# Kernel optimization log

Hardware: AMD Instinct MI355X
Metric: run time of the kernel (lower is better)

The kernel has to match this reference:

```python
import jax, jax.numpy as jnp
import numpy as np

N, C_IN, H, W = 8, 32, 64, 64
C_OUT, KH, KW = 64, 3, 3
STRIDE, PADDING = 1, 1


def setup_inputs() -> dict:
    key = jax.random.key(0)
    k1, k2 = jax.random.split(key)
    x = jax.random.normal(k1, (N, C_IN, H, W), dtype=jnp.float32)
    # kaiming_normal_ on (OC, IC, KH, KW): std = sqrt(2 / fan_in), fan_in = IC*KH*KW
    std = (2.0 / (C_IN * KH * KW)) ** 0.5
    weight = jax.random.normal(k2, (C_OUT, C_IN, KH, KW), dtype=jnp.float32) * std
    return {"x": x, "weight": weight}


def _aeg_conv2d(x, weight, stride=STRIDE, padding=PADDING):
    n, c_in, h, w = x.shape
    oc, ic, kh, kw = weight.shape
    xp = jnp.pad(x, ((0, 0), (0, 0), (padding, padding), (padding, padding)))
    oh = (h - kh + 2 * padding) // stride + 1
    ow = (w - kw + 2 * padding) // stride + 1
    K = kh * kw
    # Extract patches with static slices (KH,KW small): ps[k] has shape (N, IC, OH, OW)
    ps = jnp.stack(
        [xp[:, :, dh:dh + (oh - 1) * stride + 1:stride, dw:dw + (ow - 1) * stride + 1:stride]
         for dh in range(kh) for dw in range(kw)], axis=0)  # (K, N, IC, OH, OW)
    ws = weight.reshape(oc, ic, K).transpose(2, 0, 1)        # (K, OC, IC)
    base = jnp.arange(oh)[:, None] + jnp.arange(ow)[None, :]  # i + j, shape (OH, OW)

    def step(r, inp):
        xk, yk, k = inp
        xk = xk[:, None]                       # (N, 1, IC, OH, OW)
        yk = yk[None, :, :, None, None]        # (1, OC, IC, 1, 1)
        even = ((base + k) % 2) == 0           # (OH, OW) parity of i+j+k
        # even: r = (r + x) * y ; odd: r = (r + y) * x  (matches aeg_integrate)
        r = jnp.where(even, (r + xk) * yk, (r + yk) * xk)
        return r, None

    r0 = jnp.zeros((n, oc, ic, oh, ow), dtype=x.dtype)
    r, _ = jax.lax.scan(step, r0, (ps, ws, jnp.arange(K)))
    return r.sum(axis=2)  # sum over input channels -> (N, OC, OH, OW)


def reference(x, weight):
    return _aeg_conv2d(x, weight)
```

## Files before the change

### kernel.cpp

```cpp
#include <hip/hip_runtime.h>
#include <hip/hip_bf16.h>

#define C_IN  32
#define C_OUT 64
#define HH    64
#define WW    64

typedef __attribute__((ext_vector_type(8))) short short8v;
typedef __attribute__((ext_vector_type(4))) float f32x4;

static __device__ __forceinline__ unsigned short f2bf(float f) {
    unsigned u = __builtin_bit_cast(unsigned, f);
    unsigned r = (u + 0x7FFFu + ((u >> 16) & 1u)) >> 16;
    return (unsigned short)r;
}
static __device__ __forceinline__ float bf2f(unsigned short b) {
    unsigned u = ((unsigned)b) << 16;
    return __builtin_bit_cast(float, u);
}

#define XS_IC   273
#define XS_ROW  68
#define XS_PAR  34

template<int P>
__device__ __forceinline__ void packB(const float* __restrict__ w,
                                      short8v* __restrict__ B16, int tid)
{
    int oct  = tid >> 6;
    int lane = tid & 63;
    int oc   = oct * 16 + (lane & 15);
    int icb  = (lane >> 4) * 8;

    float wv[72];
    const f32x4* src = (const f32x4*)(w + ((size_t)oc * C_IN + icb) * 9);
    #pragma unroll
    for (int i = 0; i < 18; ++i) {
        f32x4 v = src[i];
        wv[4 * i + 0] = v.x; wv[4 * i + 1] = v.y;
        wv[4 * i + 2] = v.z; wv[4 * i + 3] = v.w;
    }

    #pragma unroll
    for (int a = 0; a < 8; ++a) {
        float Ew = 1.f;
        #pragma unroll
        for (int k = 8; k >= 0; --k) {
            float wk = wv[9 * a + k];
            if (((P + k) & 1) == 0) { Ew *= wk; wv[9 * a + k] = Ew; }
            else                    { wv[9 * a + k] = wk * Ew; }
        }
    }

    #pragma unroll
    for (int k = 0; k < 9; ++k) {
        short8v vh;
        #pragma unroll
        for (int a = 0; a < 8; ++a)
            vh[a] = (short)f2bf(wv[9 * a + k]);
        B16[(k * 4 + oct) * 64 + lane] = vh;
    }
}

template<int P>
__device__ __forceinline__ void aeg_gemm(
    float (&xt)[8][9], const short8v* __restrict__ Bq, f32x4 (&acc)[4], int l)
{
    #pragma unroll
    for (int a = 0; a < 8; ++a) {
        float Ox = 1.f;
        #pragma unroll
        for (int k = 8; k >= 0; --k) {
            if (((P + k) & 1) == 1) { Ox *= xt[a][k]; xt[a][k] = Ox; }
            else                    { xt[a][k] = xt[a][k] * Ox; }
        }
    }

    #pragma unroll
    for (int t = 0; t < 4; ++t) acc[t] = (f32x4){0.f, 0.f, 0.f, 0.f};

    #pragma unroll
    for (int k = 0; k < 9; ++k) {
        short8v ah, al;
        #pragma unroll
        for (int a = 0; a < 8; ++a) {
            float v  = xt[a][k];
            __hip_bfloat16 bh = __float2bfloat16(v);
            float fh = __bfloat162float(bh);
            __hip_bfloat16 bl = __float2bfloat16(v - fh);
            ah[a] = (short)__builtin_bit_cast(unsigned short, bh);
            al[a] = (short)__builtin_bit_cast(unsigned short, bl);
        }
        #pragma unroll
        for (int t = 0; t < 4; ++t) {
            short8v bh = Bq[(k * 4 + t) * 64 + l];
            acc[t] = __builtin_amdgcn_mfma_f32_16x16x32_bf16(ah, bh, acc[t], 0, 0, 0);
            acc[t] = __builtin_amdgcn_mfma_f32_16x16x32_bf16(al, bh, acc[t], 0, 0, 0);
        }
    }
}

__global__ __launch_bounds__(256, 2) void aeg_mfma(
    const float* __restrict__ x, const float* __restrict__ w,
    float* __restrict__ out)
{
    __shared__ __attribute__((aligned(16))) unsigned short Blds[18432];
    __shared__ float xs[C_IN * XS_IC];

    int bid = blockIdx.x;
    int pp  = bid & 1;
    int br  = (bid >> 1) & 31;
    int n   = bid >> 6;
    int i0  = br * 2;
    int tid = threadIdx.x;

    {
        const float* xn = x + (size_t)n * C_IN * HH * WW;
        #pragma unroll
        for (int c8 = 0; c8 < 8; ++c8) {
            int chunk = c8 * 256 + tid;
            int ic  = chunk >> 6;
            int row = (chunk >> 4) & 3;
            int cv  = chunk & 15;
            int ii  = i0 - 1 + row;
            f32x4 v = (f32x4){0.f, 0.f, 0.f, 0.f};
            if ((unsigned)ii < 64u)
                v = *(const f32x4*)(xn + ((size_t)ic * HH + ii) * WW + cv * 4);
            float* dstp = xs + ic * XS_IC + row * XS_ROW;
            dstp[0 * XS_PAR + 2 * cv + 1] = v.x;
            dstp[1 * XS_PAR + 2 * cv + 1] = v.y;
            dstp[0 * XS_PAR + 2 * cv + 2] = v.z;
            dstp[1 * XS_PAR + 2 * cv + 2] = v.w;
        }
        int ic  = tid >> 3;
        int row = (tid >> 1) & 3;
        float* dstp = xs + ic * XS_IC + row * XS_ROW;
        if (tid & 1) dstp[1 * XS_PAR + 0]  = 0.f;
        else         dstp[0 * XS_PAR + 33] = 0.f;
    }

    if (pp == 0) packB<0>(w, (short8v*)Blds, tid);
    else         packB<1>(w, (short8v*)Blds, tid);
    __syncthreads();

    int wvv = __builtin_amdgcn_readfirstlane(tid >> 6);
    int grp = wvv;
    int l   = tid & 63;

    int qA = grp * 16 + (l & 15);
    int rb = qA >> 5;
    int iA = i0 + rb;
    int pj = (iA + pp) & 1;
    int jA = 2 * (qA & 31) + pj;
    int icb = (l >> 4) * 8;

    int slotS = ((jA - 1) >> 1) + 1;
    int slotC = (jA >> 1) + 1;
    const float* xbase = xs + icb * XS_IC;

    float xt[8][9];
    #pragma unroll
    for (int a = 0; a < 8; ++a) {
        const float* pa = xbase + a * XS_IC;
        #pragma unroll
        for (int di = 0; di < 3; ++di) {
            const float* pr = pa + (rb + di) * XS_ROW;
            xt[a][di * 3 + 0] = pr[(1 - pj) * XS_PAR + slotS];
            xt[a][di * 3 + 2] = pr[(1 - pj) * XS_PAR + slotS + 1];
            xt[a][di * 3 + 1] = pr[pj * XS_PAR + slotC];
        }
    }

    const short8v* Bq = (const short8v*)Blds;
    f32x4 acc[4];
    if (pp == 0) aeg_gemm<0>(xt, Bq, acc, l);
    else         aeg_gemm<1>(xt, Bq, acc, l);

    __syncthreads();
    float* cls = (float*)Blds;

    {
        int colc = l & 15;
        int rgrp = l >> 4;
        #pragma unroll
        for (int t = 0; t < 4; ++t) {
            int oc = t * 16 + colc;
            #pragma unroll
            for (int r = 0; r < 4; ++r) {
                int q = grp * 16 + rgrp * 4 + r;
                cls[oc * 65 + q] = acc[t][r];
            }
        }
    }
    __syncthreads();

    #pragma unroll
    for (int v = 0; v < 16; ++v) {
        int flat = v * 256 + tid;
        int oc   = flat >> 6;
        int q    = flat & 63;
        int i    = i0 + (q >> 5);
        int j    = 2 * (q & 31) + ((i + pp) & 1);
        out[(((size_t)n * C_OUT + oc) * HH + i) * WW + j] = cls[oc * 65 + q];
    }
}

extern "C" void kernel_launch(void* const* d_in, const int* in_sizes, int n_in,
                              void* d_out, int out_size, void* d_ws, size_t ws_size,
                              hipStream_t stream) {
    const float* x = (const float*)d_in[0];
    const float* w = (const float*)d_in[1];
    float* out = (float*)d_out;
    (void)d_ws; (void)ws_size;

    aeg_mfma<<<512, 256, 0, stream>>>(x, w, out);
}
```

Baseline: 18.62 us.

## Merge both parity blocks into one 512-thread block sharing the input tile

Each 512-thread block now handles both output parities for a row pair. Previously two separate blocks each loaded the same input tile. Half the threads pack the even-parity weights and half pack the odd-parity weights into a doubled LDS buffer, and the output staging is widened so that stores cover full contiguous rows. This halves redundant input loads and makes global writes contiguous. In exchange the grid drops to 256 blocks with larger LDS use per block, which may lower occupancy.

```diff
diff --git a/kernel.cpp b/kernel.cpp
--- a/kernel.cpp
+++ b/kernel.cpp
@@ -14,10 +14,6 @@
     unsigned r = (u + 0x7FFFu + ((u >> 16) & 1u)) >> 16;
     return (unsigned short)r;
 }
-static __device__ __forceinline__ float bf2f(unsigned short b) {
-    unsigned u = ((unsigned)b) << 16;
-    return __builtin_bit_cast(float, u);
-}
 
 #define XS_IC   273
 #define XS_ROW  68
@@ -25,10 +21,10 @@
 
 template<int P>
 __device__ __forceinline__ void packB(const float* __restrict__ w,
-                                      short8v* __restrict__ B16, int tid)
+                                      short8v* __restrict__ B16, int tt)
 {
-    int oct  = tid >> 6;
-    int lane = tid & 63;
+    int oct  = tt >> 6;
+    int lane = tt & 63;
     int oc   = oct * 16 + (lane & 15);
     int icb  = (lane >> 4) * 8;
 
@@ -58,7 +54,7 @@
         #pragma unroll
         for (int a = 0; a < 8; ++a)
             vh[a] = (short)f2bf(wv[9 * a + k]);
-        B16[(k * 4 + oct) * 64 + lane] = vh;
+        B16[P * 2304 + (k * 4 + oct) * 64 + lane] = vh;
     }
 }
 
@@ -100,25 +96,24 @@
     }
 }
 
-__global__ __launch_bounds__(256, 2) void aeg_mfma(
+__global__ __launch_bounds__(512, 2) void aeg_mfma(
     const float* __restrict__ x, const float* __restrict__ w,
     float* __restrict__ out)
 {
-    __shared__ __attribute__((aligned(16))) unsigned short Blds[18432];
+    __shared__ __attribute__((aligned(16))) unsigned short Blds[36864];
     __shared__ float xs[C_IN * XS_IC];
 
     int bid = blockIdx.x;
-    int pp  = bid & 1;
-    int br  = (bid >> 1) & 31;
-    int n   = bid >> 6;
+    int br  = bid & 31;
+    int n   = bid >> 5;
     int i0  = br * 2;
     int tid = threadIdx.x;
 
     {
         const float* xn = x + (size_t)n * C_IN * HH * WW;
         #pragma unroll
-        for (int c8 = 0; c8 < 8; ++c8) {
-            int chunk = c8 * 256 + tid;
+        for (int c4 = 0; c4 < 4; ++c4) {
+            int chunk = c4 * 512 + tid;
             int ic  = chunk >> 6;
             int row = (chunk >> 4) & 3;
             int cv  = chunk & 15;
@@ -132,19 +127,22 @@
             dstp[0 * XS_PAR + 2 * cv + 2] = v.z;
             dstp[1 * XS_PAR + 2 * cv + 2] = v.w;
         }
-        int ic  = tid >> 3;
-        int row = (tid >> 1) & 3;
-        float* dstp = xs + ic * XS_IC + row * XS_ROW;
-        if (tid & 1) dstp[1 * XS_PAR + 0]  = 0.f;
-        else         dstp[0 * XS_PAR + 33] = 0.f;
-    }
-
-    if (pp == 0) packB<0>(w, (short8v*)Blds, tid);
-    else         packB<1>(w, (short8v*)Blds, tid);
+        if (tid < 256) {
+            int ic  = tid >> 3;
+            int row = (tid >> 1) & 3;
+            float* dstp = xs + ic * XS_IC + row * XS_ROW;
+            if (tid & 1) dstp[1 * XS_PAR + 0]  = 0.f;
+            else         dstp[0 * XS_PAR + 33] = 0.f;
+        }
+    }
+
+    if (tid < 256) packB<0>(w, (short8v*)Blds, tid);
+    else           packB<1>(w, (short8v*)Blds, tid - 256);
     __syncthreads();
 
     int wvv = __builtin_amdgcn_readfirstlane(tid >> 6);
-    int grp = wvv;
+    int pp  = wvv >> 2;
+    int grp = wvv & 3;
     int l   = tid & 63;
 
     int qA = grp * 16 + (l & 15);
@@ -171,7 +169,7 @@
         }
     }
 
-    const short8v* Bq = (const short8v*)Blds;
+    const short8v* Bq = (const short8v*)Blds + pp * 2304;
     f32x4 acc[4];
     if (pp == 0) aeg_gemm<0>(xt, Bq, acc, l);
     else         aeg_gemm<1>(xt, Bq, acc, l);
@@ -188,7 +186,7 @@
             #pragma unroll
             for (int r = 0; r < 4; ++r) {
                 int q = grp * 16 + rgrp * 4 + r;
-                cls[oc * 65 + q] = acc[t][r];
+                cls[oc * 130 + pp * 64 + q] = acc[t][r];
             }
         }
     }
@@ -196,12 +194,14 @@
 
     #pragma unroll
     for (int v = 0; v < 16; ++v) {
-        int flat = v * 256 + tid;
-        int oc   = flat >> 6;
-        int q    = flat & 63;
+        int flat = v * 512 + tid;
+        int oc   = flat >> 7;
+        int rr   = flat & 127;
+        int pq   = rr >> 6;
+        int q    = rr & 63;
         int i    = i0 + (q >> 5);
-        int j    = 2 * (q & 31) + ((i + pp) & 1);
-        out[(((size_t)n * C_OUT + oc) * HH + i) * WW + j] = cls[oc * 65 + q];
+        int j    = 2 * (q & 31) + ((i + pq) & 1);
+        out[(((size_t)n * C_OUT + oc) * HH + i) * WW + j] = cls[oc * 130 + pq * 64 + q];
     }
 }
 
@@ -213,5 +213,5 @@
     float* out = (float*)d_out;
     (void)d_ws; (void)ws_size;
 
-    aeg_mfma<<<512, 256, 0, stream>>>(x, w, out);
-}
+    aeg_mfma<<<256, 512, 0, stream>>>(x, w, out);
+}
```

New measurement: 17.08 us. 1.09x faster.
